# Kernel optimization log

Hardware: AMD Instinct MI355X
Metric: run time of the kernel (lower is better)

## Reference

```python
import jax, jax.numpy as jnp
import numpy as np

H = 1024       # hidden_size
NH = 16        # num_attention_heads
HD = H // NH   # attention_head_size = 64


def setup_inputs() -> dict:
    key = jax.random.key(0)
    ks = jax.random.split(key, 9)
    s = 1.0 / np.sqrt(H)
    return {
        "hidden_states": jax.random.normal(ks[0], (2, 2048, H), dtype=jnp.float32),
        "Wq": jax.random.uniform(ks[1], (H, H), jnp.float32, -s, s),
        "bq": jax.random.uniform(ks[2], (H,), jnp.float32, -s, s),
        "Wk": jax.random.uniform(ks[3], (H, H), jnp.float32, -s, s),
        "bk": jax.random.uniform(ks[4], (H,), jnp.float32, -s, s),
        "Wv": jax.random.uniform(ks[5], (H, H), jnp.float32, -s, s),
        "bv": jax.random.uniform(ks[6], (H,), jnp.float32, -s, s),
        "Wo": jax.random.uniform(ks[7], (H, H), jnp.float32, -s, s),
        "bo": jax.random.uniform(ks[8], (H,), jnp.float32, -s, s),
    }


def _heads(x, B, S):
    # [B, S, H] -> [B, NH, S, HD]
    return x.reshape(B, S, NH, HD).transpose(0, 2, 1, 3)


def reference(hidden_states, Wq, bq, Wk, bk, Wv, bv, Wo, bo):
    B, S, _ = hidden_states.shape
    q = _heads(hidden_states @ Wq.T + bq, B, S)
    k = _heads(hidden_states @ Wk.T + bk, B, S)
    v = _heads(hidden_states @ Wv.T + bv, B, S)
    scores = jnp.einsum('bhqd,bhkd->bhqk', q, k) / jnp.sqrt(jnp.float32(HD))
    probs = jax.nn.softmax(scores, axis=-1)
    ctx = jnp.einsum('bhqk,bhkd->bhqd', probs, v)  # [B, NH, S, HD]
    ctx = ctx.transpose(0, 2, 1, 3).reshape(B, S, H)
    return ctx @ Wo.T + bo
```

## Files before the change

kernel.cpp:

```cpp
#include <hip/hip_runtime.h>
#include <stdint.h>


#define HH 1024
#define NHEAD 16
#define HDIM 64
#define SEQ 2048
#define NB 2
#define MTOT (NB * SEQ)
#define QSCALE 0.1803368801111204f
#define BK 32

typedef unsigned short u16;
typedef __attribute__((ext_vector_type(8))) short bf16x8;
typedef __attribute__((ext_vector_type(4))) float f32x4;

static __device__ __forceinline__ float exp2_raw(float x) {
  float r; asm("v_exp_f32 %0, %1" : "=v"(r) : "v"(x)); return r;
}
static __device__ __forceinline__ uint32_t cvtpk_bf16(float lo, float hi) {
  uint32_t r; asm("v_cvt_pk_bf16_f32 %0, %1, %2" : "=v"(r) : "v"(lo), "v"(hi)); return r;
}
static __device__ __forceinline__ void gload16(const u16* g, u16* l) {
  __builtin_amdgcn_global_load_lds(
      (const __attribute__((address_space(1))) uint32_t*)(const void*)g,
      (__attribute__((address_space(3))) uint32_t*)(void*)l, 16, 0, 0);
}
#define VMW(N) asm volatile("s_waitcnt vmcnt(" #N ")" ::: "memory")
static __device__ __forceinline__ void bar() {
  asm volatile("" ::: "memory");
  __builtin_amdgcn_s_barrier();
  asm volatile("" ::: "memory");
}

#define SWZ(row, col) (((row) * 64) + ((col) ^ (((row) & 7) << 3)))

__global__ void cvt_all_kernel(const float* __restrict__ hs,
                               const float* __restrict__ w0, const float* __restrict__ w1,
                               const float* __restrict__ w2, const float* __restrict__ w3,
                               u16* __restrict__ Xb, u16* __restrict__ Wall) {
  const int z = blockIdx.y;
  int i = blockIdx.x * 256 + threadIdx.x;
  const float* s; u16* d; int n4;
  if (z == 0) { s = hs; d = Xb; n4 = MTOT * HH / 4; }
  else {
    s = (z == 1) ? w0 : (z == 2) ? w1 : (z == 3) ? w2 : w3;
    d = Wall + (size_t)(z - 1) * HH * HH; n4 = HH * HH / 4;
  }
  if (i >= n4) return;
  float4 v = reinterpret_cast<const float4*>(s)[i];
  uint2 o;
  o.x = cvtpk_bf16(v.x, v.y);
  o.y = cvtpk_bf16(v.z, v.w);
  reinterpret_cast<uint2*>(d)[i] = o;
}

__global__ __launch_bounds__(256, 3)
void gemm_qkv_kernel(const u16* __restrict__ A, const u16* __restrict__ W,
                     const float* __restrict__ bq, const float* __restrict__ bk,
                     const float* __restrict__ bv,
                     u16* __restrict__ outQ, u16* __restrict__ outK, u16* __restrict__ outVT)
{
  const int tid  = threadIdx.x;
  const int lane = tid & 63, wave = tid >> 6;
  const int wm = wave >> 1, wn = wave & 1;
  const int l15 = lane & 15, l4 = lane >> 4;
  const int brow = blockIdx.x * 128, bcol = blockIdx.y * 128;

  __shared__ __align__(16) u16 lA[3][128 * BK];
  __shared__ __align__(16) u16 lB[3][128 * BK];

  const int sr = wave * 16 + (lane >> 2);
  const int sc = (lane & 3) ^ ((sr >> 1) & 3);
  const u16* gA0 = A + (size_t)(brow + sr) * HH + sc * 8;
  const u16* gA1 = A + (size_t)(brow + sr + 64) * HH + sc * 8;
  const u16* gB0 = W + (size_t)(bcol + sr) * HH + sc * 8;
  const u16* gB1 = W + (size_t)(bcol + sr + 64) * HH + sc * 8;

#define STAGEQ(slot, kt)                                                      \
  { gload16(gA0 + (kt) * BK, (u16*)((char*)&lA[slot][0] + wave * 1024));      \
    gload16(gA1 + (kt) * BK, (u16*)((char*)&lA[slot][0] + 4096 + wave * 1024)); \
    gload16(gB0 + (kt) * BK, (u16*)((char*)&lB[slot][0] + wave * 1024));      \
    gload16(gB1 + (kt) * BK, (u16*)((char*)&lB[slot][0] + 4096 + wave * 1024)); }

  int aoff[4], boff[4];
#pragma unroll
  for (int mr = 0; mr < 4; ++mr) {
    int r = wm * 64 + mr * 16 + l15;
    aoff[mr] = r * BK + ((l4 ^ ((r >> 1) & 3)) * 8);
  }
#pragma unroll
  for (int nr = 0; nr < 4; ++nr) {
    int r = wn * 64 + nr * 16 + l15;
    boff[nr] = r * BK + ((l4 ^ ((r >> 1) & 3)) * 8);
  }

  f32x4 acc[4][4];
#pragma unroll
  for (int mr = 0; mr < 4; ++mr)
#pragma unroll
    for (int nr = 0; nr < 4; ++nr) acc[mr][nr] = (f32x4){0.f, 0.f, 0.f, 0.f};

  STAGEQ(0, 0);
  STAGEQ(1, 1);

  for (int k = 0; k < 32; ++k) {
    if (k < 31) VMW(4); else VMW(0);
    bar();

    if (k + 2 < 32) STAGEQ((k + 2) % 3, k + 2);

    const u16* sA = &lA[k % 3][0];
    const u16* sB = &lB[k % 3][0];
    bf16x8 a[4], b[4];
#pragma unroll
    for (int nr = 0; nr < 4; ++nr) b[nr] = *reinterpret_cast<const bf16x8*>(sB + boff[nr]);
#pragma unroll
    for (int mr = 0; mr < 4; ++mr) a[mr] = *reinterpret_cast<const bf16x8*>(sA + aoff[mr]);

    __builtin_amdgcn_s_setprio(1);
#pragma unroll
    for (int mr = 0; mr < 4; ++mr)
#pragma unroll
      for (int nr = 0; nr < 4; ++nr)
        acc[mr][nr] = __builtin_amdgcn_mfma_f32_16x16x32_bf16(a[mr], b[nr], acc[mr][nr], 0, 0, 0);
    __builtin_amdgcn_s_setprio(0);
  }
#undef STAGEQ

  const int mode = bcol >> 10;
#pragma unroll
  for (int mr = 0; mr < 4; ++mr) {
    int m0 = brow + wm * 64 + mr * 16 + l4 * 4;
    int bb = m0 >> 11, s0 = m0 & (SEQ - 1);
#pragma unroll
    for (int nr = 0; nr < 4; ++nr) {
      int n = bcol + wn * 64 + nr * 16 + l15;
      int nn = n & (HH - 1);
      int h = nn >> 6, d = nn & (HDIM - 1);
      float bias_n = (mode == 0) ? bq[nn] : (mode == 1) ? bk[nn] : bv[nn];
      if (mode == 2) {
        int p0 = (s0 & ~31) | (((s0 >> 2) & 3) << 3) | (((s0 >> 4) & 1) << 2);
        uint2 pk4;
        pk4.x = cvtpk_bf16(acc[mr][nr][0] + bias_n, acc[mr][nr][1] + bias_n);
        pk4.y = cvtpk_bf16(acc[mr][nr][2] + bias_n, acc[mr][nr][3] + bias_n);
        *reinterpret_cast<uint2*>(&outVT[((size_t)(bb * NHEAD + h) * HDIM + d) * SEQ + p0]) = pk4;
      } else {
        u16* dst = (mode == 0) ? outQ : outK;
        float sc2 = (mode == 0) ? QSCALE : 1.0f;
        uint32_t r01 = cvtpk_bf16((acc[mr][nr][0] + bias_n) * sc2, (acc[mr][nr][1] + bias_n) * sc2);
        uint32_t r23 = cvtpk_bf16((acc[mr][nr][2] + bias_n) * sc2, (acc[mr][nr][3] + bias_n) * sc2);
        size_t base = ((size_t)(bb * NHEAD + h) * SEQ + s0) * HDIM + d;
        dst[base]            = (u16)r01;
        dst[base + HDIM]     = (u16)(r01 >> 16);
        dst[base + 2 * HDIM] = (u16)r23;
        dst[base + 3 * HDIM] = (u16)(r23 >> 16);
      }
    }
  }
}

__global__ __launch_bounds__(512, 4)
void gemm_o_kernel(const u16* __restrict__ A, const u16* __restrict__ W,
                   const float* __restrict__ bo, float* __restrict__ outF)
{
  const int tid  = threadIdx.x;
  const int lane = tid & 63, wave = tid >> 6;
  const int wm = wave >> 1, wn = wave & 1;
  const int l15 = lane & 15, l4 = lane >> 4;
  const int brow = blockIdx.x * 128, bcol = blockIdx.y * 128;

  __shared__ __align__(16) u16 lA[4][128 * BK];
  __shared__ __align__(16) u16 lB[4][128 * BK];

  const int sr = wave * 16 + (lane >> 2);
  const int sc = (lane & 3) ^ ((sr >> 1) & 3);
  const u16* gA = A + (size_t)(brow + sr) * HH + sc * 8;
  const u16* gB = W + (size_t)(bcol + sr) * HH + sc * 8;

  int aoff[2], boff[4];
#pragma unroll
  for (int mr = 0; mr < 2; ++mr) {
    int r = wm * 32 + mr * 16 + l15;
    aoff[mr] = r * BK + ((l4 ^ ((r >> 1) & 3)) * 8);
  }
#pragma unroll
  for (int nr = 0; nr < 4; ++nr) {
    int r = wn * 64 + nr * 16 + l15;
    boff[nr] = r * BK + ((l4 ^ ((r >> 1) & 3)) * 8);
  }

  f32x4 acc[2][4];
#pragma unroll
  for (int mr = 0; mr < 2; ++mr)
#pragma unroll
    for (int nr = 0; nr < 4; ++nr) acc[mr][nr] = (f32x4){0.f, 0.f, 0.f, 0.f};

#pragma unroll
  for (int t = 0; t < 3; ++t) {
    gload16(gA + t * BK, (u16*)((char*)&lA[t][0] + wave * 1024));
    gload16(gB + t * BK, (u16*)((char*)&lB[t][0] + wave * 1024));
  }

  for (int k = 0; k < 32; ++k) {
    const int rem = 31 - k;
    if (rem >= 2)      VMW(4);
    else if (rem == 1) VMW(2);
    else               VMW(0);
    bar();

    const int s = k & 3, tt = (k + 3) & 3;
    if (k + 3 < 32) {
      gload16(gA + (k + 3) * BK, (u16*)((char*)&lA[tt][0] + wave * 1024));
      gload16(gB + (k + 3) * BK, (u16*)((char*)&lB[tt][0] + wave * 1024));
    }

    const u16* sA = &lA[s][0];
    const u16* sB = &lB[s][0];
    bf16x8 a[2], b[4];
#pragma unroll
    for (int nr = 0; nr < 4; ++nr) b[nr] = *reinterpret_cast<const bf16x8*>(sB + boff[nr]);
#pragma unroll
    for (int mr = 0; mr < 2; ++mr) a[mr] = *reinterpret_cast<const bf16x8*>(sA + aoff[mr]);

    __builtin_amdgcn_s_setprio(1);
#pragma unroll
    for (int mr = 0; mr < 2; ++mr)
#pragma unroll
      for (int nr = 0; nr < 4; ++nr)
        acc[mr][nr] = __builtin_amdgcn_mfma_f32_16x16x32_bf16(a[mr], b[nr], acc[mr][nr], 0, 0, 0);
    __builtin_amdgcn_s_setprio(0);
  }

#pragma unroll
  for (int mr = 0; mr < 2; ++mr) {
    int m0 = brow + wm * 32 + mr * 16 + l4 * 4;
#pragma unroll
    for (int nr = 0; nr < 4; ++nr) {
      int n = bcol + wn * 64 + nr * 16 + l15;
      float bias_n = bo[n];
#pragma unroll
      for (int t = 0; t < 4; ++t)
        outF[(size_t)(m0 + t) * HH + n] = acc[mr][nr][t] + bias_n;
    }
  }
}

__global__ __launch_bounds__(256)
void attn_kernel(const u16* __restrict__ Qh, const u16* __restrict__ Kh,
                 const u16* __restrict__ VTh, u16* __restrict__ CTX)
{
  const int head = blockIdx.x;
  const int qb   = blockIdx.y;
  const int tid  = threadIdx.x;
  const int lane = tid & 63, wave = tid >> 6;
  const int l15 = lane & 15, l4 = lane >> 4;

  __shared__ __align__(16) u16 lK[2][64 * 64];
  __shared__ __align__(16) u16 lV[2][64 * 64];

  const u16* Qg = Qh + ((size_t)head * SEQ + qb * 128 + wave * 32) * HDIM;
  const u16* Kg = Kh + (size_t)head * SEQ * HDIM;
  const u16* Vg = VTh + (size_t)head * HDIM * SEQ;

  const int srow = wave * 16 + (lane >> 3);
  const int scol = ((lane & 7) ^ (lane >> 3)) * 8;
  const u16* gk0 = Kg + (size_t)srow * HDIM + scol;
  const u16* gk1 = gk0 + 8 * HDIM;
  const u16* gv0 = Vg + (size_t)srow * SEQ + scol;
  const u16* gv1 = gv0 + 8 * SEQ;

#define ASTAGE(buf, kt)                                                   \
  { gload16(gk0 + (size_t)(kt) * 64 * HDIM, &lK[buf][(wave * 2 + 0) * 512]); \
    gload16(gk1 + (size_t)(kt) * 64 * HDIM, &lK[buf][(wave * 2 + 1) * 512]); \
    gload16(gv0 + (kt) * 64,                &lV[buf][(wave * 2 + 0) * 512]); \
    gload16(gv1 + (kt) * 64,                &lV[buf][(wave * 2 + 1) * 512]); }

  bf16x8 qf[2][2];
#pragma unroll
  for (int g = 0; g < 2; ++g)
#pragma unroll
    for (int kk = 0; kk < 2; ++kk)
      qf[g][kk] = *reinterpret_cast<const bf16x8*>(&Qg[(g * 16 + l15) * HDIM + kk * 32 + l4 * 8]);

  int kfi[2][4], vfi[2][4];
#pragma unroll
  for (int kk = 0; kk < 2; ++kk)
#pragma unroll
    for (int j = 0; j < 4; ++j) {
      kfi[kk][j] = SWZ(j * 16 + l15, kk * 32 + l4 * 8);
      vfi[kk][j] = SWZ(j * 16 + l15, kk * 32 + l4 * 8);
    }

  ASTAGE(0, 0);
  __syncthreads();

  union { uint32_t u[4]; bf16x8 v; } ones;
#pragma unroll
  for (int t = 0; t < 4; ++t) ones.u[t] = 0x3F803F80u;

  f32x4 accO[2][4];
  f32x4 accS[2];
#pragma unroll
  for (int g = 0; g < 2; ++g) {
#pragma unroll
    for (int dj = 0; dj < 4; ++dj) accO[g][dj] = (f32x4){0.f, 0.f, 0.f, 0.f};
    accS[g] = (f32x4){0.f, 0.f, 0.f, 0.f};
  }

  for (int kb = 0; kb < SEQ / 64; ++kb) {
    const int cur = kb & 1;
    const bool pre = (kb + 1 < SEQ / 64);
    if (pre) ASTAGE(cur ^ 1, kb + 1);

    bf16x8 kf[2][4];
#pragma unroll
    for (int kk = 0; kk < 2; ++kk)
#pragma unroll
      for (int kj = 0; kj < 4; ++kj)
        kf[kk][kj] = *reinterpret_cast<const bf16x8*>(&lK[cur][kfi[kk][kj]]);

    union { uint32_t u[4]; bf16x8 v; } pfr[2][2];
#pragma unroll
    for (int g = 0; g < 2; ++g) {
      f32x4 sf[4];
#pragma unroll
      for (int kj = 0; kj < 4; ++kj) sf[kj] = (f32x4){0.f, 0.f, 0.f, 0.f};
      __builtin_amdgcn_s_setprio(1);
#pragma unroll
      for (int kk = 0; kk < 2; ++kk)
#pragma unroll
        for (int kj = 0; kj < 4; ++kj)
          sf[kj] = __builtin_amdgcn_mfma_f32_16x16x32_bf16(kf[kk][kj], qf[g][kk], sf[kj], 0, 0, 0);
      __builtin_amdgcn_s_setprio(0);
#pragma unroll
      for (int kj = 0; kj < 4; ++kj) {
        float p0 = exp2_raw(sf[kj][0]);
        float p1 = exp2_raw(sf[kj][1]);
        float p2 = exp2_raw(sf[kj][2]);
        float p3 = exp2_raw(sf[kj][3]);
        pfr[g][kj >> 1].u[(kj & 1) * 2 + 0] = cvtpk_bf16(p0, p1);
        pfr[g][kj >> 1].u[(kj & 1) * 2 + 1] = cvtpk_bf16(p2, p3);
      }
    }

#pragma unroll
    for (int kk = 0; kk < 2; ++kk) {
      bf16x8 vf[4];
#pragma unroll
      for (int dj = 0; dj < 4; ++dj)
        vf[dj] = *reinterpret_cast<const bf16x8*>(&lV[cur][vfi[kk][dj]]);
      __builtin_amdgcn_s_setprio(1);
#pragma unroll
      for (int g = 0; g < 2; ++g) {
#pragma unroll
        for (int dj = 0; dj < 4; ++dj)
          accO[g][dj] = __builtin_amdgcn_mfma_f32_16x16x32_bf16(vf[dj], pfr[g][kk].v, accO[g][dj], 0, 0, 0);
        accS[g] = __builtin_amdgcn_mfma_f32_16x16x32_bf16(ones.v, pfr[g][kk].v, accS[g], 0, 0, 0);
      }
      __builtin_amdgcn_s_setprio(0);
    }

    if (pre) __syncthreads();
  }
#undef ASTAGE

  const int bb = head >> 4, h = head & (NHEAD - 1);
#pragma unroll
  for (int g = 0; g < 2; ++g) {
    const int sq = qb * 128 + wave * 32 + g * 16 + l15;
    float inv = 1.0f / accS[g][0];
#pragma unroll
    for (int dj = 0; dj < 4; ++dj) {
      uint2 o;
      o.x = cvtpk_bf16(accO[g][dj][0] * inv, accO[g][dj][1] * inv);
      o.y = cvtpk_bf16(accO[g][dj][2] * inv, accO[g][dj][3] * inv);
      *reinterpret_cast<uint2*>(&CTX[((size_t)(bb * SEQ + sq)) * HH + h * HDIM + dj * 16 + l4 * 4]) = o;
    }
  }
}

extern "C" void kernel_launch(void* const* d_in, const int* in_sizes, int n_in,
                              void* d_out, int out_size, void* d_ws, size_t ws_size,
                              hipStream_t stream) {
  const float* hs = (const float*)d_in[0];
  const float* Wq = (const float*)d_in[1];
  const float* bq = (const float*)d_in[2];
  const float* Wk = (const float*)d_in[3];
  const float* bk = (const float*)d_in[4];
  const float* Wv = (const float*)d_in[5];
  const float* bv = (const float*)d_in[6];
  const float* Wo = (const float*)d_in[7];
  const float* bo = (const float*)d_in[8];
  float* out = (float*)d_out;

  char* ws = (char*)d_ws;
  u16* Xb   = (u16*)(ws);
  u16* Wall = (u16*)(ws + ((size_t)8 << 20));
  u16* Qh   = (u16*)(ws + ((size_t)16 << 20));
  u16* Kh   = (u16*)(ws + ((size_t)24 << 20));
  u16* VT   = (u16*)(ws + ((size_t)32 << 20));
  u16* CT   = Xb;

  cvt_all_kernel<<<dim3(MTOT * HH / 4 / 256, 5), 256, 0, stream>>>(
      hs, Wq, Wk, Wv, Wo, Xb, Wall);

  gemm_qkv_kernel<<<dim3(MTOT / 128, 3 * HH / 128), 256, 0, stream>>>(
      Xb, Wall, bq, bk, bv, Qh, Kh, VT);

  attn_kernel<<<dim3(NB * NHEAD, SEQ / 128), 256, 0, stream>>>(Qh, Kh, VT, CT);

  gemm_o_kernel<<<dim3(MTOT / 128, HH / 128), 512, 0, stream>>>(
      CT, Wall + (size_t)3 * HH * HH, bo, out);
}
```

Before: 110.7 us.

## Software-pipeline attention, retile O-projection GEMM, flatten conversion grid

The attention loop is reorganised to process key blocks in pairs with ping-pong probability registers. The PV product of the previous block overlaps the QK^T/exp of the next, and V gets triple buffering. The output GEMM moves from 512 to 256 threads per block, each wave computing a 64x64 tile with a 3-stage LDS ring instead of 4. The conversion kernel switches to a flat 1D grid that packs X and all weights contiguously, so no blocks go idle on the small weight planes. These changes aim to hide LDS/global latency and reduce wasted launch work, at the cost of more registers per wave and more complex synchronisation.

Result: faster. 108.1 us (-2.4%).

```diff
diff --git a/kernel.cpp b/kernel.cpp
--- a/kernel.cpp
+++ b/kernel.cpp
@@ -38,21 +38,22 @@
 __global__ void cvt_all_kernel(const float* __restrict__ hs,
                                const float* __restrict__ w0, const float* __restrict__ w1,
                                const float* __restrict__ w2, const float* __restrict__ w3,
-                               u16* __restrict__ Xb, u16* __restrict__ Wall) {
-  const int z = blockIdx.y;
+                               u16* __restrict__ dst) {
+  const int NX = MTOT * HH / 4;
+  const int NW = HH * HH / 4;
   int i = blockIdx.x * 256 + threadIdx.x;
-  const float* s; u16* d; int n4;
-  if (z == 0) { s = hs; d = Xb; n4 = MTOT * HH / 4; }
+  const float* s; int j;
+  if (i < NX) { s = hs; j = i; }
   else {
-    s = (z == 1) ? w0 : (z == 2) ? w1 : (z == 3) ? w2 : w3;
-    d = Wall + (size_t)(z - 1) * HH * HH; n4 = HH * HH / 4;
-  }
-  if (i >= n4) return;
-  float4 v = reinterpret_cast<const float4*>(s)[i];
+    int w = (i - NX) >> 18;
+    j = (i - NX) & (NW - 1);
+    s = (w == 0) ? w0 : (w == 1) ? w1 : (w == 2) ? w2 : w3;
+  }
+  float4 v = reinterpret_cast<const float4*>(s)[j];
   uint2 o;
   o.x = cvtpk_bf16(v.x, v.y);
   o.y = cvtpk_bf16(v.z, v.w);
-  reinterpret_cast<uint2*>(d)[i] = o;
+  reinterpret_cast<uint2*>(dst)[i] = o;
 }
 
 __global__ __launch_bounds__(256, 3)
@@ -160,7 +161,7 @@
   }
 }
 
-__global__ __launch_bounds__(512, 4)
+__global__ __launch_bounds__(256, 3)
 void gemm_o_kernel(const u16* __restrict__ A, const u16* __restrict__ W,
                    const float* __restrict__ bo, float* __restrict__ outF)
 {
@@ -170,18 +171,26 @@
   const int l15 = lane & 15, l4 = lane >> 4;
   const int brow = blockIdx.x * 128, bcol = blockIdx.y * 128;
 
-  __shared__ __align__(16) u16 lA[4][128 * BK];
-  __shared__ __align__(16) u16 lB[4][128 * BK];
+  __shared__ __align__(16) u16 lA[3][128 * BK];
+  __shared__ __align__(16) u16 lB[3][128 * BK];
 
   const int sr = wave * 16 + (lane >> 2);
   const int sc = (lane & 3) ^ ((sr >> 1) & 3);
-  const u16* gA = A + (size_t)(brow + sr) * HH + sc * 8;
-  const u16* gB = W + (size_t)(bcol + sr) * HH + sc * 8;
-
-  int aoff[2], boff[4];
-#pragma unroll
-  for (int mr = 0; mr < 2; ++mr) {
-    int r = wm * 32 + mr * 16 + l15;
+  const u16* gA0 = A + (size_t)(brow + sr) * HH + sc * 8;
+  const u16* gA1 = A + (size_t)(brow + sr + 64) * HH + sc * 8;
+  const u16* gB0 = W + (size_t)(bcol + sr) * HH + sc * 8;
+  const u16* gB1 = W + (size_t)(bcol + sr + 64) * HH + sc * 8;
+
+#define STAGEO(slot, kt)                                                      \
+  { gload16(gA0 + (kt) * BK, (u16*)((char*)&lA[slot][0] + wave * 1024));      \
+    gload16(gA1 + (kt) * BK, (u16*)((char*)&lA[slot][0] + 4096 + wave * 1024)); \
+    gload16(gB0 + (kt) * BK, (u16*)((char*)&lB[slot][0] + wave * 1024));      \
+    gload16(gB1 + (kt) * BK, (u16*)((char*)&lB[slot][0] + 4096 + wave * 1024)); }
+
+  int aoff[4], boff[4];
+#pragma unroll
+  for (int mr = 0; mr < 4; ++mr) {
+    int r = wm * 64 + mr * 16 + l15;
     aoff[mr] = r * BK + ((l4 ^ ((r >> 1) & 3)) * 8);
   }
 #pragma unroll
@@ -190,51 +199,42 @@
     boff[nr] = r * BK + ((l4 ^ ((r >> 1) & 3)) * 8);
   }
 
-  f32x4 acc[2][4];
-#pragma unroll
-  for (int mr = 0; mr < 2; ++mr)
+  f32x4 acc[4][4];
+#pragma unroll
+  for (int mr = 0; mr < 4; ++mr)
 #pragma unroll
     for (int nr = 0; nr < 4; ++nr) acc[mr][nr] = (f32x4){0.f, 0.f, 0.f, 0.f};
 
-#pragma unroll
-  for (int t = 0; t < 3; ++t) {
-    gload16(gA + t * BK, (u16*)((char*)&lA[t][0] + wave * 1024));
-    gload16(gB + t * BK, (u16*)((char*)&lB[t][0] + wave * 1024));
-  }
+  STAGEO(0, 0);
+  STAGEO(1, 1);
 
   for (int k = 0; k < 32; ++k) {
-    const int rem = 31 - k;
-    if (rem >= 2)      VMW(4);
-    else if (rem == 1) VMW(2);
-    else               VMW(0);
+    if (k < 31) VMW(4); else VMW(0);
     bar();
 
-    const int s = k & 3, tt = (k + 3) & 3;
-    if (k + 3 < 32) {
-      gload16(gA + (k + 3) * BK, (u16*)((char*)&lA[tt][0] + wave * 1024));
-      gload16(gB + (k + 3) * BK, (u16*)((char*)&lB[tt][0] + wave * 1024));
-    }
-
-    const u16* sA = &lA[s][0];
-    const u16* sB = &lB[s][0];
-    bf16x8 a[2], b[4];
+    if (k + 2 < 32) STAGEO((k + 2) % 3, k + 2);
+
+    const u16* sA = &lA[k % 3][0];
+    const u16* sB = &lB[k % 3][0];
+    bf16x8 a[4], b[4];
 #pragma unroll
     for (int nr = 0; nr < 4; ++nr) b[nr] = *reinterpret_cast<const bf16x8*>(sB + boff[nr]);
 #pragma unroll
-    for (int mr = 0; mr < 2; ++mr) a[mr] = *reinterpret_cast<const bf16x8*>(sA + aoff[mr]);
+    for (int mr = 0; mr < 4; ++mr) a[mr] = *reinterpret_cast<const bf16x8*>(sA + aoff[mr]);
 
     __builtin_amdgcn_s_setprio(1);
 #pragma unroll
-    for (int mr = 0; mr < 2; ++mr)
+    for (int mr = 0; mr < 4; ++mr)
 #pragma unroll
       for (int nr = 0; nr < 4; ++nr)
         acc[mr][nr] = __builtin_amdgcn_mfma_f32_16x16x32_bf16(a[mr], b[nr], acc[mr][nr], 0, 0, 0);
     __builtin_amdgcn_s_setprio(0);
   }
-
-#pragma unroll
-  for (int mr = 0; mr < 2; ++mr) {
-    int m0 = brow + wm * 32 + mr * 16 + l4 * 4;
+#undef STAGEO
+
+#pragma unroll
+  for (int mr = 0; mr < 4; ++mr) {
+    int m0 = brow + wm * 64 + mr * 16 + l4 * 4;
 #pragma unroll
     for (int nr = 0; nr < 4; ++nr) {
       int n = bcol + wn * 64 + nr * 16 + l15;
@@ -257,7 +257,7 @@
   const int l15 = lane & 15, l4 = lane >> 4;
 
   __shared__ __align__(16) u16 lK[2][64 * 64];
-  __shared__ __align__(16) u16 lV[2][64 * 64];
+  __shared__ __align__(16) u16 lV[3][64 * 64];
 
   const u16* Qg = Qh + ((size_t)head * SEQ + qb * 128 + wave * 32) * HDIM;
   const u16* Kg = Kh + (size_t)head * SEQ * HDIM;
@@ -270,11 +270,12 @@
   const u16* gv0 = Vg + (size_t)srow * SEQ + scol;
   const u16* gv1 = gv0 + 8 * SEQ;
 
-#define ASTAGE(buf, kt)                                                   \
-  { gload16(gk0 + (size_t)(kt) * 64 * HDIM, &lK[buf][(wave * 2 + 0) * 512]); \
-    gload16(gk1 + (size_t)(kt) * 64 * HDIM, &lK[buf][(wave * 2 + 1) * 512]); \
-    gload16(gv0 + (kt) * 64,                &lV[buf][(wave * 2 + 0) * 512]); \
-    gload16(gv1 + (kt) * 64,                &lV[buf][(wave * 2 + 1) * 512]); }
+#define KSTAGE(buf, kt)                                                       \
+  { gload16(gk0 + (size_t)(kt) * 64 * HDIM, &lK[buf][(wave * 2 + 0) * 512]);  \
+    gload16(gk1 + (size_t)(kt) * 64 * HDIM, &lK[buf][(wave * 2 + 1) * 512]); }
+#define VSTAGE(buf, kt)                                                       \
+  { gload16(gv0 + (kt) * 64, &lV[buf][(wave * 2 + 0) * 512]);                 \
+    gload16(gv1 + (kt) * 64, &lV[buf][(wave * 2 + 1) * 512]); }
 
   bf16x8 qf[2][2];
 #pragma unroll
@@ -283,16 +284,14 @@
     for (int kk = 0; kk < 2; ++kk)
       qf[g][kk] = *reinterpret_cast<const bf16x8*>(&Qg[(g * 16 + l15) * HDIM + kk * 32 + l4 * 8]);
 
-  int kfi[2][4], vfi[2][4];
+  int fi[2][4];
 #pragma unroll
   for (int kk = 0; kk < 2; ++kk)
 #pragma unroll
-    for (int j = 0; j < 4; ++j) {
-      kfi[kk][j] = SWZ(j * 16 + l15, kk * 32 + l4 * 8);
-      vfi[kk][j] = SWZ(j * 16 + l15, kk * 32 + l4 * 8);
-    }
-
-  ASTAGE(0, 0);
+    for (int j = 0; j < 4; ++j)
+      fi[kk][j] = SWZ(j * 16 + l15, kk * 32 + l4 * 8);
+
+  KSTAGE(0, 0); VSTAGE(0, 0);
   __syncthreads();
 
   union { uint32_t u[4]; bf16x8 v; } ones;
@@ -308,62 +307,77 @@
     accS[g] = (f32x4){0.f, 0.f, 0.f, 0.f};
   }
 
-  for (int kb = 0; kb < SEQ / 64; ++kb) {
-    const int cur = kb & 1;
-    const bool pre = (kb + 1 < SEQ / 64);
-    if (pre) ASTAGE(cur ^ 1, kb + 1);
-
-    bf16x8 kf[2][4];
-#pragma unroll
-    for (int kk = 0; kk < 2; ++kk)
-#pragma unroll
-      for (int kj = 0; kj < 4; ++kj)
-        kf[kk][kj] = *reinterpret_cast<const bf16x8*>(&lK[cur][kfi[kk][kj]]);
-
-    union { uint32_t u[4]; bf16x8 v; } pfr[2][2];
-#pragma unroll
-    for (int g = 0; g < 2; ++g) {
-      f32x4 sf[4];
-#pragma unroll
-      for (int kj = 0; kj < 4; ++kj) sf[kj] = (f32x4){0.f, 0.f, 0.f, 0.f};
-      __builtin_amdgcn_s_setprio(1);
-#pragma unroll
-      for (int kk = 0; kk < 2; ++kk)
-#pragma unroll
-        for (int kj = 0; kj < 4; ++kj)
-          sf[kj] = __builtin_amdgcn_mfma_f32_16x16x32_bf16(kf[kk][kj], qf[g][kk], sf[kj], 0, 0, 0);
-      __builtin_amdgcn_s_setprio(0);
-#pragma unroll
-      for (int kj = 0; kj < 4; ++kj) {
-        float p0 = exp2_raw(sf[kj][0]);
-        float p1 = exp2_raw(sf[kj][1]);
-        float p2 = exp2_raw(sf[kj][2]);
-        float p3 = exp2_raw(sf[kj][3]);
-        pfr[g][kj >> 1].u[(kj & 1) * 2 + 0] = cvtpk_bf16(p0, p1);
-        pfr[g][kj >> 1].u[(kj & 1) * 2 + 1] = cvtpk_bf16(p2, p3);
-      }
-    }
-
-#pragma unroll
-    for (int kk = 0; kk < 2; ++kk) {
-      bf16x8 vf[4];
-#pragma unroll
-      for (int dj = 0; dj < 4; ++dj)
-        vf[dj] = *reinterpret_cast<const bf16x8*>(&lV[cur][vfi[kk][dj]]);
-      __builtin_amdgcn_s_setprio(1);
-#pragma unroll
-      for (int g = 0; g < 2; ++g) {
-#pragma unroll
-        for (int dj = 0; dj < 4; ++dj)
-          accO[g][dj] = __builtin_amdgcn_mfma_f32_16x16x32_bf16(vf[dj], pfr[g][kk].v, accO[g][dj], 0, 0, 0);
-        accS[g] = __builtin_amdgcn_mfma_f32_16x16x32_bf16(ones.v, pfr[g][kk].v, accS[g], 0, 0, 0);
-      }
-      __builtin_amdgcn_s_setprio(0);
-    }
-
-    if (pre) __syncthreads();
-  }
-#undef ASTAGE
+  union PU { uint32_t u[4]; bf16x8 v; };
+  PU pfrA[2][2], pfrB[2][2];
+
+#define QKT_EXP(PFR, kbuf)                                                    \
+  {                                                                           \
+    bf16x8 kf[2][4];                                                          \
+    _Pragma("unroll")                                                         \
+    for (int kk = 0; kk < 2; ++kk)                                            \
+      _Pragma("unroll")                                                       \
+      for (int kj = 0; kj < 4; ++kj)                                          \
+        kf[kk][kj] = *reinterpret_cast<const bf16x8*>(&lK[kbuf][fi[kk][kj]]); \
+    _Pragma("unroll")                                                         \
+    for (int g = 0; g < 2; ++g) {                                             \
+      f32x4 sf[4];                                                            \
+      _Pragma("unroll")                                                       \
+      for (int kj = 0; kj < 4; ++kj) sf[kj] = (f32x4){0.f, 0.f, 0.f, 0.f};    \
+      __builtin_amdgcn_s_setprio(1);                                          \
+      _Pragma("unroll")                                                       \
+      for (int kk = 0; kk < 2; ++kk)                                          \
+        _Pragma("unroll")                                                     \
+        for (int kj = 0; kj < 4; ++kj)                                        \
+          sf[kj] = __builtin_amdgcn_mfma_f32_16x16x32_bf16(kf[kk][kj], qf[g][kk], sf[kj], 0, 0, 0); \
+      __builtin_amdgcn_s_setprio(0);                                          \
+      _Pragma("unroll")                                                       \
+      for (int kj = 0; kj < 4; ++kj) {                                        \
+        float p0 = exp2_raw(sf[kj][0]);                                       \
+        float p1 = exp2_raw(sf[kj][1]);                                       \
+        float p2 = exp2_raw(sf[kj][2]);                                       \
+        float p3 = exp2_raw(sf[kj][3]);                                       \
+        PFR[g][kj >> 1].u[(kj & 1) * 2 + 0] = cvtpk_bf16(p0, p1);             \
+        PFR[g][kj >> 1].u[(kj & 1) * 2 + 1] = cvtpk_bf16(p2, p3);             \
+      }                                                                       \
+    }                                                                         \
+  }
+
+#define PV(PFR, vslot)                                                        \
+  {                                                                           \
+    _Pragma("unroll")                                                         \
+    for (int kk = 0; kk < 2; ++kk) {                                          \
+      bf16x8 vf[4];                                                           \
+      _Pragma("unroll")                                                       \
+      for (int dj = 0; dj < 4; ++dj)                                          \
+        vf[dj] = *reinterpret_cast<const bf16x8*>(&lV[vslot][fi[kk][dj]]);    \
+      __builtin_amdgcn_s_setprio(1);                                          \
+      _Pragma("unroll")                                                       \
+      for (int g = 0; g < 2; ++g) {                                           \
+        _Pragma("unroll")                                                     \
+        for (int dj = 0; dj < 4; ++dj)                                        \
+          accO[g][dj] = __builtin_amdgcn_mfma_f32_16x16x32_bf16(vf[dj], PFR[g][kk].v, accO[g][dj], 0, 0, 0); \
+        accS[g] = __builtin_amdgcn_mfma_f32_16x16x32_bf16(ones.v, PFR[g][kk].v, accS[g], 0, 0, 0); \
+      }                                                                       \
+      __builtin_amdgcn_s_setprio(0);                                          \
+    }                                                                         \
+  }
+
+  for (int kp = 0; kp < 16; ++kp) {
+    const int k0 = 2 * kp, k1 = k0 + 1;
+    KSTAGE(1, k1); VSTAGE(k1 % 3, k1);
+    QKT_EXP(pfrA, 0);
+    if (kp > 0) PV(pfrB, (k0 - 1) % 3);
+    __syncthreads();
+    if (k1 + 1 < 32) { KSTAGE(0, k1 + 1); VSTAGE((k1 + 1) % 3, k1 + 1); }
+    QKT_EXP(pfrB, 1);
+    PV(pfrA, k0 % 3);
+    if (k1 + 1 < 32) __syncthreads();
+  }
+  PV(pfrB, 31 % 3);
+#undef QKT_EXP
+#undef PV
+#undef KSTAGE
+#undef VSTAGE
 
   const int bb = head >> 4, h = head & (NHEAD - 1);
 #pragma unroll
@@ -402,14 +416,15 @@
   u16* VT   = (u16*)(ws + ((size_t)32 << 20));
   u16* CT   = Xb;
 
-  cvt_all_kernel<<<dim3(MTOT * HH / 4 / 256, 5), 256, 0, stream>>>(
-      hs, Wq, Wk, Wv, Wo, Xb, Wall);
+  const int nflt4 = MTOT * HH / 4 + HH * HH;
+  cvt_all_kernel<<<dim3(nflt4 / 256), 256, 0, stream>>>(
+      hs, Wq, Wk, Wv, Wo, (u16*)ws);
 
   gemm_qkv_kernel<<<dim3(MTOT / 128, 3 * HH / 128), 256, 0, stream>>>(
       Xb, Wall, bq, bk, bv, Qh, Kh, VT);
 
   attn_kernel<<<dim3(NB * NHEAD, SEQ / 128), 256, 0, stream>>>(Qh, Kh, VT, CT);
 
-  gemm_o_kernel<<<dim3(MTOT / 128, HH / 128), 512, 0, stream>>>(
+  gemm_o_kernel<<<dim3(MTOT / 128, HH / 128), 256, 0, stream>>>(
       CT, Wall + (size_t)3 * HH * HH, bo, out);
 }
```

## Shrink attention and output-GEMM tiles and flatten the conversion grid

Applied to the files above, without the earlier changes.

The conversion kernel becomes a flat 1D grid that writes X and all four weights contiguously into the workspace, which removes the idle blocks of the old 5-row grid where the weight rows were mostly empty. The attention kernel moves to 128 threads with 64 query rows per block, doubling the block count for better CU occupancy, but each block now loads the same K/V per fewer queries. The output GEMM uses 64x128 tiles with 256 threads and a 3-stage pipeline instead of 128x128 with 512 threads and 4 stages, giving more blocks to spread across CUs.

Result: no change. 109.3 us (-1.3%).

```diff
diff --git a/kernel.cpp b/kernel.cpp
--- a/kernel.cpp
+++ b/kernel.cpp
@@ -38,21 +38,22 @@
 __global__ void cvt_all_kernel(const float* __restrict__ hs,
                                const float* __restrict__ w0, const float* __restrict__ w1,
                                const float* __restrict__ w2, const float* __restrict__ w3,
-                               u16* __restrict__ Xb, u16* __restrict__ Wall) {
-  const int z = blockIdx.y;
+                               u16* __restrict__ dst) {
+  const int NX = MTOT * HH / 4;
+  const int NW = HH * HH / 4;
   int i = blockIdx.x * 256 + threadIdx.x;
-  const float* s; u16* d; int n4;
-  if (z == 0) { s = hs; d = Xb; n4 = MTOT * HH / 4; }
+  const float* s; int j;
+  if (i < NX) { s = hs; j = i; }
   else {
-    s = (z == 1) ? w0 : (z == 2) ? w1 : (z == 3) ? w2 : w3;
-    d = Wall + (size_t)(z - 1) * HH * HH; n4 = HH * HH / 4;
-  }
-  if (i >= n4) return;
-  float4 v = reinterpret_cast<const float4*>(s)[i];
+    int w = (i - NX) >> 18;
+    j = (i - NX) & (NW - 1);
+    s = (w == 0) ? w0 : (w == 1) ? w1 : (w == 2) ? w2 : w3;
+  }
+  float4 v = reinterpret_cast<const float4*>(s)[j];
   uint2 o;
   o.x = cvtpk_bf16(v.x, v.y);
   o.y = cvtpk_bf16(v.z, v.w);
-  reinterpret_cast<uint2*>(d)[i] = o;
+  reinterpret_cast<uint2*>(dst)[i] = o;
 }
 
 __global__ __launch_bounds__(256, 3)
@@ -160,7 +161,7 @@
   }
 }
 
-__global__ __launch_bounds__(512, 4)
+__global__ __launch_bounds__(256, 3)
 void gemm_o_kernel(const u16* __restrict__ A, const u16* __restrict__ W,
                    const float* __restrict__ bo, float* __restrict__ outF)
 {
@@ -168,15 +169,22 @@
   const int lane = tid & 63, wave = tid >> 6;
   const int wm = wave >> 1, wn = wave & 1;
   const int l15 = lane & 15, l4 = lane >> 4;
-  const int brow = blockIdx.x * 128, bcol = blockIdx.y * 128;
-
-  __shared__ __align__(16) u16 lA[4][128 * BK];
-  __shared__ __align__(16) u16 lB[4][128 * BK];
-
-  const int sr = wave * 16 + (lane >> 2);
-  const int sc = (lane & 3) ^ ((sr >> 1) & 3);
-  const u16* gA = A + (size_t)(brow + sr) * HH + sc * 8;
-  const u16* gB = W + (size_t)(bcol + sr) * HH + sc * 8;
+  const int brow = blockIdx.x * 64, bcol = blockIdx.y * 128;
+
+  __shared__ __align__(16) u16 lA[3][64 * BK];
+  __shared__ __align__(16) u16 lB[3][128 * BK];
+
+  const int ra = wave * 16 + (lane >> 2);
+  const u16* gAo = A + (size_t)(brow + ra) * HH + (((lane & 3) ^ ((ra >> 1) & 3)) * 8);
+  const int rb0 = (wave * 2 + 0) * 16 + (lane >> 2);
+  const int rb1 = (wave * 2 + 1) * 16 + (lane >> 2);
+  const u16* gBo0 = W + (size_t)(bcol + rb0) * HH + (((lane & 3) ^ ((rb0 >> 1) & 3)) * 8);
+  const u16* gBo1 = W + (size_t)(bcol + rb1) * HH + (((lane & 3) ^ ((rb1 >> 1) & 3)) * 8);
+
+#define STAGEO(slot, kt)                                                      \
+  { gload16(gAo  + (kt) * BK, &lA[slot][wave * 512]);                         \
+    gload16(gBo0 + (kt) * BK, &lB[slot][(wave * 2 + 0) * 512]);               \
+    gload16(gBo1 + (kt) * BK, &lB[slot][(wave * 2 + 1) * 512]); }
 
   int aoff[2], boff[4];
 #pragma unroll
@@ -196,27 +204,17 @@
 #pragma unroll
     for (int nr = 0; nr < 4; ++nr) acc[mr][nr] = (f32x4){0.f, 0.f, 0.f, 0.f};
 
-#pragma unroll
-  for (int t = 0; t < 3; ++t) {
-    gload16(gA + t * BK, (u16*)((char*)&lA[t][0] + wave * 1024));
-    gload16(gB + t * BK, (u16*)((char*)&lB[t][0] + wave * 1024));
-  }
+  STAGEO(0, 0);
+  STAGEO(1, 1);
 
   for (int k = 0; k < 32; ++k) {
-    const int rem = 31 - k;
-    if (rem >= 2)      VMW(4);
-    else if (rem == 1) VMW(2);
-    else               VMW(0);
+    if (k < 31) VMW(3); else VMW(0);
     bar();
 
-    const int s = k & 3, tt = (k + 3) & 3;
-    if (k + 3 < 32) {
-      gload16(gA + (k + 3) * BK, (u16*)((char*)&lA[tt][0] + wave * 1024));
-      gload16(gB + (k + 3) * BK, (u16*)((char*)&lB[tt][0] + wave * 1024));
-    }
-
-    const u16* sA = &lA[s][0];
-    const u16* sB = &lB[s][0];
+    if (k + 2 < 32) STAGEO((k + 2) % 3, k + 2);
+
+    const u16* sA = &lA[k % 3][0];
+    const u16* sB = &lB[k % 3][0];
     bf16x8 a[2], b[4];
 #pragma unroll
     for (int nr = 0; nr < 4; ++nr) b[nr] = *reinterpret_cast<const bf16x8*>(sB + boff[nr]);
@@ -231,6 +229,7 @@
         acc[mr][nr] = __builtin_amdgcn_mfma_f32_16x16x32_bf16(a[mr], b[nr], acc[mr][nr], 0, 0, 0);
     __builtin_amdgcn_s_setprio(0);
   }
+#undef STAGEO
 
 #pragma unroll
   for (int mr = 0; mr < 2; ++mr) {
@@ -246,7 +245,7 @@
   }
 }
 
-__global__ __launch_bounds__(256)
+__global__ __launch_bounds__(128)
 void attn_kernel(const u16* __restrict__ Qh, const u16* __restrict__ Kh,
                  const u16* __restrict__ VTh, u16* __restrict__ CTX)
 {
@@ -259,22 +258,27 @@
   __shared__ __align__(16) u16 lK[2][64 * 64];
   __shared__ __align__(16) u16 lV[2][64 * 64];
 
-  const u16* Qg = Qh + ((size_t)head * SEQ + qb * 128 + wave * 32) * HDIM;
+  const u16* Qg = Qh + ((size_t)head * SEQ + qb * 64 + wave * 32) * HDIM;
   const u16* Kg = Kh + (size_t)head * SEQ * HDIM;
   const u16* Vg = VTh + (size_t)head * HDIM * SEQ;
 
-  const int srow = wave * 16 + (lane >> 3);
   const int scol = ((lane & 7) ^ (lane >> 3)) * 8;
-  const u16* gk0 = Kg + (size_t)srow * HDIM + scol;
-  const u16* gk1 = gk0 + 8 * HDIM;
-  const u16* gv0 = Vg + (size_t)srow * SEQ + scol;
-  const u16* gv1 = gv0 + 8 * SEQ;
-
-#define ASTAGE(buf, kt)                                                   \
-  { gload16(gk0 + (size_t)(kt) * 64 * HDIM, &lK[buf][(wave * 2 + 0) * 512]); \
-    gload16(gk1 + (size_t)(kt) * 64 * HDIM, &lK[buf][(wave * 2 + 1) * 512]); \
-    gload16(gv0 + (kt) * 64,                &lV[buf][(wave * 2 + 0) * 512]); \
-    gload16(gv1 + (kt) * 64,                &lV[buf][(wave * 2 + 1) * 512]); }
+  const u16* gk[4]; const u16* gv[4];
+#pragma unroll
+  for (int i = 0; i < 4; ++i) {
+    int r = wave * 32 + i * 8 + (lane >> 3);
+    gk[i] = Kg + (size_t)r * HDIM + scol;
+    gv[i] = Vg + (size_t)r * SEQ + scol;
+  }
+
+#define KSTAGE(buf, kt)                                                       \
+  { _Pragma("unroll")                                                         \
+    for (int i = 0; i < 4; ++i)                                               \
+      gload16(gk[i] + (size_t)(kt) * 64 * HDIM, &lK[buf][(wave * 4 + i) * 512]); }
+#define VSTAGE(buf, kt)                                                       \
+  { _Pragma("unroll")                                                         \
+    for (int i = 0; i < 4; ++i)                                               \
+      gload16(gv[i] + (kt) * 64, &lV[buf][(wave * 4 + i) * 512]); }
 
   bf16x8 qf[2][2];
 #pragma unroll
@@ -283,16 +287,14 @@
     for (int kk = 0; kk < 2; ++kk)
       qf[g][kk] = *reinterpret_cast<const bf16x8*>(&Qg[(g * 16 + l15) * HDIM + kk * 32 + l4 * 8]);
 
-  int kfi[2][4], vfi[2][4];
+  int fi[2][4];
 #pragma unroll
   for (int kk = 0; kk < 2; ++kk)
 #pragma unroll
-    for (int j = 0; j < 4; ++j) {
-      kfi[kk][j] = SWZ(j * 16 + l15, kk * 32 + l4 * 8);
-      vfi[kk][j] = SWZ(j * 16 + l15, kk * 32 + l4 * 8);
-    }
-
-  ASTAGE(0, 0);
+    for (int j = 0; j < 4; ++j)
+      fi[kk][j] = SWZ(j * 16 + l15, kk * 32 + l4 * 8);
+
+  KSTAGE(0, 0); VSTAGE(0, 0);
   __syncthreads();
 
   union { uint32_t u[4]; bf16x8 v; } ones;
@@ -311,14 +313,14 @@
   for (int kb = 0; kb < SEQ / 64; ++kb) {
     const int cur = kb & 1;
     const bool pre = (kb + 1 < SEQ / 64);
-    if (pre) ASTAGE(cur ^ 1, kb + 1);
+    if (pre) { KSTAGE(cur ^ 1, kb + 1); VSTAGE(cur ^ 1, kb + 1); }
 
     bf16x8 kf[2][4];
 #pragma unroll
     for (int kk = 0; kk < 2; ++kk)
 #pragma unroll
       for (int kj = 0; kj < 4; ++kj)
-        kf[kk][kj] = *reinterpret_cast<const bf16x8*>(&lK[cur][kfi[kk][kj]]);
+        kf[kk][kj] = *reinterpret_cast<const bf16x8*>(&lK[cur][fi[kk][kj]]);
 
     union { uint32_t u[4]; bf16x8 v; } pfr[2][2];
 #pragma unroll
@@ -349,7 +351,7 @@
       bf16x8 vf[4];
 #pragma unroll
       for (int dj = 0; dj < 4; ++dj)
-        vf[dj] = *reinterpret_cast<const bf16x8*>(&lV[cur][vfi[kk][dj]]);
+        vf[dj] = *reinterpret_cast<const bf16x8*>(&lV[cur][fi[kk][dj]]);
       __builtin_amdgcn_s_setprio(1);
 #pragma unroll
       for (int g = 0; g < 2; ++g) {
@@ -363,12 +365,13 @@
 
     if (pre) __syncthreads();
   }
-#undef ASTAGE
+#undef KSTAGE
+#undef VSTAGE
 
   const int bb = head >> 4, h = head & (NHEAD - 1);
 #pragma unroll
   for (int g = 0; g < 2; ++g) {
-    const int sq = qb * 128 + wave * 32 + g * 16 + l15;
+    const int sq = qb * 64 + wave * 32 + g * 16 + l15;
     float inv = 1.0f / accS[g][0];
 #pragma unroll
     for (int dj = 0; dj < 4; ++dj) {
@@ -402,14 +405,15 @@
   u16* VT   = (u16*)(ws + ((size_t)32 << 20));
   u16* CT   = Xb;
 
-  cvt_all_kernel<<<dim3(MTOT * HH / 4 / 256, 5), 256, 0, stream>>>(
-      hs, Wq, Wk, Wv, Wo, Xb, Wall);
+  const int nflt4 = MTOT * HH / 4 + HH * HH;
+  cvt_all_kernel<<<dim3(nflt4 / 256), 256, 0, stream>>>(
+      hs, Wq, Wk, Wv, Wo, (u16*)ws);
 
   gemm_qkv_kernel<<<dim3(MTOT / 128, 3 * HH / 128), 256, 0, stream>>>(
       Xb, Wall, bq, bk, bv, Qh, Kh, VT);
 
-  attn_kernel<<<dim3(NB * NHEAD, SEQ / 128), 256, 0, stream>>>(Qh, Kh, VT, CT);
-
-  gemm_o_kernel<<<dim3(MTOT / 128, HH / 128), 512, 0, stream>>>(
+  attn_kernel<<<dim3(NB * NHEAD, SEQ / 64), 128, 0, stream>>>(Qh, Kh, VT, CT);
+
+  gemm_o_kernel<<<dim3(MTOT / 64, HH / 128), 256, 0, stream>>>(
       CT, Wall + (size_t)3 * HH * HH, bo, out);
 }
```
